# Kernel tuning notes

Measured on AMD Instinct MI355X. Metric: run time of the kernel, lower is better.

The kernel has to match this reference:

```python
import jax, jax.numpy as jnp
import numpy as np

BATCH = 131072
S = 128  # state_size == x_size


def setup_inputs() -> dict:
    key = jax.random.key(0)
    ks = jax.random.split(key, 7)
    std = 1.0 / np.sqrt(S).astype(np.float32)
    return {
        "x": jax.random.normal(ks[0], (BATCH, S), dtype=jnp.float32),
        "old_h": jax.random.normal(ks[1], (BATCH, S), dtype=jnp.float32),
        "W_x1": jax.random.normal(ks[2], (3, S, S), dtype=jnp.float32) * std,
        "W_x2": jax.random.normal(ks[3], (3, S, S), dtype=jnp.float32) * std,
        "W_h": jax.random.normal(ks[4], (6, S, S), dtype=jnp.float32) * std,
        "b": jnp.zeros((6, 1, S), dtype=jnp.float32),
        "mid": jax.random.normal(ks[5], (S, S), dtype=jnp.float32) * std,
    }


def reference(x, old_h, W_x1, W_x2, W_h, b, mid):
    sg = jax.nn.sigmoid
    # --- first GRU stage ---
    z = sg(x @ W_x1[0] + old_h @ W_h[0] + b[0])
    r = sg(x @ W_x1[1] + old_h @ W_h[1] + b[1])
    h_tilde = jnp.tanh(x @ W_x1[2] + (r * old_h) @ W_h[2] + b[2])
    mid_h = z * old_h + (1.0 - z) * h_tilde
    # mid_dropout with p=0 is identity
    mid_x = jax.nn.relu(mid_h @ mid)
    # --- second GRU stage (faithfully reuses W_h[0], b[0] as in source) ---
    z2 = sg(mid_x @ W_x2[0] + mid_h @ W_h[0] + b[0])
    r2 = sg(mid_x @ W_x2[1] + mid_h @ W_h[4] + b[4])
    h2_tilde = jnp.tanh(mid_x @ W_x2[2] + (r2 * mid_h) @ W_h[5] + b[5])
    h = z2 * mid_h + (1.0 - z2) * h2_tilde
    return (h,)
```

## Files before the change

kernel.cpp:

```cpp
#include <hip/hip_runtime.h>
#include <hip/hip_bf16.h>
#include <cstdint>


typedef __attribute__((ext_vector_type(8))) short bf16x8;
typedef __attribute__((ext_vector_type(4))) float f32x4;

#define S 128
#define BM 64
#define THREADS 512

#define SWZB(row) (((((row) & 7) ^ (((row) >> 2) & 2))) << 4)

__device__ __forceinline__ unsigned short f2bf(float f) {
    __hip_bfloat16 h = __float2bfloat16(f);
    return *reinterpret_cast<unsigned short*>(&h);
}
__device__ __forceinline__ float bf2f(unsigned short h) {
    unsigned int u = ((unsigned int)h) << 16;
    return __builtin_bit_cast(float, u);
}

__device__ __forceinline__ float fast_sig(float t) {
    float e = __expf(-t);
    return __builtin_amdgcn_rcpf(1.0f + e);
}
__device__ __forceinline__ float fast_tanh(float t) {
    float tc = fminf(fmaxf(t, -15.0f), 15.0f);
    float e = __expf(2.0f * tc);
    return (e - 1.0f) * __builtin_amdgcn_rcpf(e + 1.0f);
}

__global__ void pack_weights(const float* __restrict__ wx1,
                             const float* __restrict__ wx2,
                             const float* __restrict__ wh,
                             const float* __restrict__ mid,
                             unsigned short* __restrict__ dst) {
    int mat = blockIdx.x;
    const float* src;
    if (mat < 3)       src = wx1 + mat * (S * S);
    else if (mat < 6)  src = wx2 + (mat - 3) * (S * S);
    else if (mat < 12) src = wh  + (mat - 6) * (S * S);
    else               src = mid;
    int t = threadIdx.x;
    for (int f8 = 0; f8 < 8; ++f8) {
        int slot = f8 * 256 + t;
        int frag = slot >> 6;
        int lane = slot & 63;
        int kt  = frag >> 3;
        int ntg = frag & 7;
        int k0  = kt * 32 + (lane >> 4) * 8;
        int col = ntg * 16 + (lane & 15);
        unsigned int w[4];
#pragma unroll
        for (int p = 0; p < 4; ++p) {
            unsigned int lo = f2bf(src[(k0 + 2 * p) * S + col]);
            unsigned int hi = f2bf(src[(k0 + 2 * p + 1) * S + col]);
            w[p] = lo | (hi << 16);
        }
        uint4* d = (uint4*)(dst + (size_t)mat * (S * S) + frag * 512 + lane * 8);
        *d = make_uint4(w[0], w[1], w[2], w[3]);
    }
}

__device__ __forceinline__ bf16x8 lds_afrag(const unsigned short* s, int row, int kt, int lane) {
    int byte = row * 256 + kt * 64 + ((lane >> 4) << 4);
    byte ^= SWZB(row);
    return *(const bf16x8*)((const char*)s + byte);
}
__device__ __forceinline__ void st_bf(unsigned short* s, int row, int col, float v) {
    int byte = (row * 256 + col * 2) ^ SWZB(row);
    *(unsigned short*)((char*)s + byte) = f2bf(v);
}
__device__ __forceinline__ float ld_bf(const unsigned short* s, int row, int col) {
    int byte = (row * 256 + col * 2) ^ SWZB(row);
    return bf2f(*(const unsigned short*)((const char*)s + byte));
}

__device__ __forceinline__ void gemm_single(f32x4 (&acc)[4],
        const unsigned short* sA,
        const unsigned short* __restrict__ w0,
        int lane, int wc) {
    int rbase = lane & 15;
    __builtin_amdgcn_s_setprio(1);
#pragma unroll
    for (int kt = 0; kt < 4; ++kt) {
        bf16x8 a0[4];
#pragma unroll
        for (int m = 0; m < 4; ++m)
            a0[m] = lds_afrag(sA, rbase + m * 16, kt, lane);
        bf16x8 b0 = *(const bf16x8*)(w0 + (kt * 8 + wc) * 512 + lane * 8);
#pragma unroll
        for (int m = 0; m < 4; ++m)
            acc[m] = __builtin_amdgcn_mfma_f32_16x16x32_bf16(a0[m], b0, acc[m], 0, 0, 0);
    }
    __builtin_amdgcn_s_setprio(0);
}

__device__ __forceinline__ void gemm_pair2(f32x4 (&acc0)[4], f32x4 (&acc1)[4],
        const unsigned short* sA,
        const unsigned short* __restrict__ w0,
        const unsigned short* __restrict__ w1,
        int lane, int wc) {
    int rbase = lane & 15;
    __builtin_amdgcn_s_setprio(1);
#pragma unroll
    for (int kt = 0; kt < 4; ++kt) {
        bf16x8 a0[4];
#pragma unroll
        for (int m = 0; m < 4; ++m)
            a0[m] = lds_afrag(sA, rbase + m * 16, kt, lane);
        bf16x8 b0 = *(const bf16x8*)(w0 + (kt * 8 + wc) * 512 + lane * 8);
        bf16x8 b1 = *(const bf16x8*)(w1 + (kt * 8 + wc) * 512 + lane * 8);
#pragma unroll
        for (int m = 0; m < 4; ++m) {
            acc0[m] = __builtin_amdgcn_mfma_f32_16x16x32_bf16(a0[m], b0, acc0[m], 0, 0, 0);
            acc1[m] = __builtin_amdgcn_mfma_f32_16x16x32_bf16(a0[m], b1, acc1[m], 0, 0, 0);
        }
    }
    __builtin_amdgcn_s_setprio(0);
}

template <int OP>
__device__ __forceinline__ void finish(f32x4 (&acc)[4], float bc) {
#pragma unroll
    for (int m = 0; m < 4; ++m)
#pragma unroll
        for (int i = 0; i < 4; ++i) {
            float t = acc[m][i] + bc;
            acc[m][i] = (OP == 0) ? fast_sig(t) : fast_tanh(t);
        }
}

#define ZERO_ACC(A)                                           \
    _Pragma("unroll") for (int m = 0; m < 4; ++m)             \
        A[m] = (f32x4){0.f, 0.f, 0.f, 0.f};

#define FOR_COORDS(BODY)                                      \
    _Pragma("unroll") for (int m = 0; m < 4; ++m)             \
    _Pragma("unroll") for (int i = 0; i < 4; ++i) {           \
        int rt  = m * 16 + ((lane >> 4) << 2) + i;            \
        int col = wc * 16 + (lane & 15);                      \
        BODY                                                  \
    }

__global__ __launch_bounds__(THREADS, 4)
void dgru_main(const float* __restrict__ x, const float* __restrict__ old_h,
               const float* __restrict__ b, const unsigned short* __restrict__ wpk,
               float* __restrict__ out) {
    __shared__ __align__(16) unsigned short sx[S * BM];
    __shared__ __align__(16) unsigned short sh[S * BM];
    __shared__ __align__(16) unsigned short sg[S * BM];

    const int tid  = threadIdx.x;
    const int lane = tid & 63;
    const int wc   = tid >> 6;
    const long row0 = (long)blockIdx.x * BM;

    float bld[6];
#pragma unroll
    for (int j = 0; j < 6; ++j)
        bld[j] = b[j * S + wc * 16 + (lane & 15)];

#pragma unroll
    for (int it = 0; it < 2; ++it) {
        int slot = it * THREADS + tid;
        int row  = slot >> 4;
        int c8   = slot & 15;
        const float4* px = (const float4*)(x     + (row0 + row) * S + c8 * 8);
        const float4* ph = (const float4*)(old_h + (row0 + row) * S + c8 * 8);
        float4 v0 = px[0], v1 = px[1];
        float4 u0 = ph[0], u1 = ph[1];
        int byte = (row * 256 + c8 * 16) ^ SWZB(row);
        uint4 wx, wh;
        wx.x = (unsigned)f2bf(v0.x) | ((unsigned)f2bf(v0.y) << 16);
        wx.y = (unsigned)f2bf(v0.z) | ((unsigned)f2bf(v0.w) << 16);
        wx.z = (unsigned)f2bf(v1.x) | ((unsigned)f2bf(v1.y) << 16);
        wx.w = (unsigned)f2bf(v1.z) | ((unsigned)f2bf(v1.w) << 16);
        wh.x = (unsigned)f2bf(u0.x) | ((unsigned)f2bf(u0.y) << 16);
        wh.y = (unsigned)f2bf(u0.z) | ((unsigned)f2bf(u0.w) << 16);
        wh.z = (unsigned)f2bf(u1.x) | ((unsigned)f2bf(u1.y) << 16);
        wh.w = (unsigned)f2bf(u1.z) | ((unsigned)f2bf(u1.w) << 16);
        *(uint4*)((char*)sx + byte) = wx;
        *(uint4*)((char*)sh + byte) = wh;
    }
    __syncthreads();

#define WP(m) (wpk + (size_t)(m) * (S * S))

    float oh[4][4];
    float mh[4][4];

    f32x4 zz[4]; ZERO_ACC(zz);
    {
        f32x4 rr[4]; ZERO_ACC(rr);
        gemm_pair2(zz, rr, sx, WP(0), WP(1), lane, wc);
        gemm_pair2(zz, rr, sh, WP(6), WP(7), lane, wc);
        finish<0>(zz, bld[0]);
        finish<0>(rr, bld[1]);
        FOR_COORDS({
            oh[m][i] = ld_bf(sh, rt, col);
            st_bf(sg, rt, col, rr[m][i] * oh[m][i]);
        })
    }
    __syncthreads();

    {
        f32x4 ht[4]; ZERO_ACC(ht);
        gemm_single(ht, sx, WP(2), lane, wc);
        gemm_single(ht, sg, WP(8), lane, wc);
        finish<1>(ht, bld[2]);
        FOR_COORDS({
            float z = zz[m][i];
            mh[m][i] = z * oh[m][i] + (1.0f - z) * ht[m][i];
            st_bf(sh, rt, col, mh[m][i]);
        })
    }
    __syncthreads();

    {
        f32x4 mx[4]; ZERO_ACC(mx);
        gemm_single(mx, sh, WP(12), lane, wc);
        FOR_COORDS({
            float v = mx[m][i];
            st_bf(sx, rt, col, v > 0.0f ? v : 0.0f);
        })
    }
    __syncthreads();

    f32x4 z2[4]; ZERO_ACC(z2);
    {
        f32x4 r2[4]; ZERO_ACC(r2);
        gemm_pair2(z2, r2, sx, WP(3), WP(4), lane, wc);
        gemm_pair2(z2, r2, sh, WP(6), WP(10), lane, wc);
        finish<0>(z2, bld[0]);
        finish<0>(r2, bld[4]);
        FOR_COORDS({
            st_bf(sg, rt, col, r2[m][i] * mh[m][i]);
        })
    }
    __syncthreads();

    {
        f32x4 h2[4]; ZERO_ACC(h2);
        gemm_single(h2, sx, WP(5), lane, wc);
        gemm_single(h2, sg, WP(11), lane, wc);
        finish<1>(h2, bld[5]);
        FOR_COORDS({
            float z = z2[m][i];
            st_bf(sh, rt, col, z * mh[m][i] + (1.0f - z) * h2[m][i]);
        })
    }
    __syncthreads();

#pragma unroll
    for (int it = 0; it < 2; ++it) {
        int slot = it * THREADS + tid;
        int row  = slot >> 4;
        int c8   = slot & 15;
        int byte = (row * 256 + c8 * 16) ^ SWZB(row);
        bf16x8 v = *(const bf16x8*)((const char*)sh + byte);
        float4 f0, f1;
        f0.x = bf2f((unsigned short)v[0]); f0.y = bf2f((unsigned short)v[1]);
        f0.z = bf2f((unsigned short)v[2]); f0.w = bf2f((unsigned short)v[3]);
        f1.x = bf2f((unsigned short)v[4]); f1.y = bf2f((unsigned short)v[5]);
        f1.z = bf2f((unsigned short)v[6]); f1.w = bf2f((unsigned short)v[7]);
        float4* po = (float4*)(out + (row0 + row) * S + c8 * 8);
        po[0] = f0;
        po[1] = f1;
    }
}

extern "C" void kernel_launch(void* const* d_in, const int* in_sizes, int n_in,
                              void* d_out, int out_size, void* d_ws, size_t ws_size,
                              hipStream_t stream) {
    const float* x     = (const float*)d_in[0];
    const float* old_h = (const float*)d_in[1];
    const float* W_x1  = (const float*)d_in[2];
    const float* W_x2  = (const float*)d_in[3];
    const float* W_h   = (const float*)d_in[4];
    const float* b     = (const float*)d_in[5];
    const float* mid   = (const float*)d_in[6];
    float* out = (float*)d_out;
    unsigned short* wpk = (unsigned short*)d_ws;

    int batch = in_sizes[0] / S;

    pack_weights<<<13, 256, 0, stream>>>(W_x1, W_x2, W_h, mid, wpk);
    dgru_main<<<batch / BM, THREADS, 0, stream>>>(x, old_h, b, wpk, out);
}
```

Before: 112.1 us.

## Switch GEMMs to 32x32x16 MFMA with 2x4 wave tiling

Replaces the 16x16x32 MFMA tiling, where each wave owned a 64x16 output strip, with 32x32x16 MFMA where each wave owns a 32x32 tile in a 2x4 wave grid. The weight packing layout changes to match the new B-fragment shape. Each wave now needs one A fragment per k-step instead of four, which cuts LDS reads and B-fragment global loads per MFMA. Intermediate old_h and mid_h values are re-read from LDS as bf16 instead of being held in registers, which lowers register pressure but uses the rounded bf16 copies and adds LDS traffic.

```diff
diff --git a/kernel.cpp b/kernel.cpp
--- a/kernel.cpp
+++ b/kernel.cpp
@@ -4,7 +4,7 @@
 
 
 typedef __attribute__((ext_vector_type(8))) short bf16x8;
-typedef __attribute__((ext_vector_type(4))) float f32x4;
+typedef __attribute__((ext_vector_type(16))) float f32x16;
 
 #define S 128
 #define BM 64
@@ -47,10 +47,10 @@
         int slot = f8 * 256 + t;
         int frag = slot >> 6;
         int lane = slot & 63;
-        int kt  = frag >> 3;
-        int ntg = frag & 7;
-        int k0  = kt * 32 + (lane >> 4) * 8;
-        int col = ntg * 16 + (lane & 15);
+        int kt  = frag >> 2;
+        int ng  = frag & 3;
+        int k0  = kt * 16 + (lane >> 5) * 8;
+        int col = ng * 32 + (lane & 31);
         unsigned int w[4];
 #pragma unroll
         for (int p = 0; p < 4; ++p) {
@@ -63,85 +63,71 @@
     }
 }
 
-__device__ __forceinline__ bf16x8 lds_afrag(const unsigned short* s, int row, int kt, int lane) {
-    int byte = row * 256 + kt * 64 + ((lane >> 4) << 4);
-    byte ^= SWZB(row);
-    return *(const bf16x8*)((const char*)s + byte);
-}
 __device__ __forceinline__ void st_bf(unsigned short* s, int row, int col, float v) {
-    int byte = (row * 256 + col * 2) ^ SWZB(row);
+    int byte = row * 256 + ((col * 2) ^ SWZB(row));
     *(unsigned short*)((char*)s + byte) = f2bf(v);
 }
 __device__ __forceinline__ float ld_bf(const unsigned short* s, int row, int col) {
-    int byte = (row * 256 + col * 2) ^ SWZB(row);
+    int byte = row * 256 + ((col * 2) ^ SWZB(row));
     return bf2f(*(const unsigned short*)((const char*)s + byte));
 }
 
-__device__ __forceinline__ void gemm_single(f32x4 (&acc)[4],
-        const unsigned short* sA,
-        const unsigned short* __restrict__ w0,
-        int lane, int wc) {
-    int rbase = lane & 15;
+__device__ __forceinline__ void gemm32(f32x16& acc, const unsigned short* sA,
+        const unsigned short* __restrict__ w0, int lane, int wr, int wcg) {
+    int row  = wr * 32 + (lane & 31);
+    int rb   = row * 256;
+    int half = (lane >> 5) << 4;
+    int swz  = SWZB(row);
+    const unsigned short* wb = w0 + wcg * 512 + lane * 8;
     __builtin_amdgcn_s_setprio(1);
 #pragma unroll
-    for (int kt = 0; kt < 4; ++kt) {
-        bf16x8 a0[4];
-#pragma unroll
-        for (int m = 0; m < 4; ++m)
-            a0[m] = lds_afrag(sA, rbase + m * 16, kt, lane);
-        bf16x8 b0 = *(const bf16x8*)(w0 + (kt * 8 + wc) * 512 + lane * 8);
-#pragma unroll
-        for (int m = 0; m < 4; ++m)
-            acc[m] = __builtin_amdgcn_mfma_f32_16x16x32_bf16(a0[m], b0, acc[m], 0, 0, 0);
+    for (int kt = 0; kt < 8; ++kt) {
+        bf16x8 a = *(const bf16x8*)((const char*)sA + rb + (((kt << 5) | half) ^ swz));
+        bf16x8 b = *(const bf16x8*)(wb + kt * 2048);
+        acc = __builtin_amdgcn_mfma_f32_32x32x16_bf16(a, b, acc, 0, 0, 0);
     }
     __builtin_amdgcn_s_setprio(0);
 }
 
-__device__ __forceinline__ void gemm_pair2(f32x4 (&acc0)[4], f32x4 (&acc1)[4],
+__device__ __forceinline__ void gemm32_pair(f32x16& acc0, f32x16& acc1,
         const unsigned short* sA,
         const unsigned short* __restrict__ w0,
         const unsigned short* __restrict__ w1,
-        int lane, int wc) {
-    int rbase = lane & 15;
+        int lane, int wr, int wcg) {
+    int row  = wr * 32 + (lane & 31);
+    int rb   = row * 256;
+    int half = (lane >> 5) << 4;
+    int swz  = SWZB(row);
+    const unsigned short* wb0 = w0 + wcg * 512 + lane * 8;
+    const unsigned short* wb1 = w1 + wcg * 512 + lane * 8;
     __builtin_amdgcn_s_setprio(1);
 #pragma unroll
-    for (int kt = 0; kt < 4; ++kt) {
-        bf16x8 a0[4];
-#pragma unroll
-        for (int m = 0; m < 4; ++m)
-            a0[m] = lds_afrag(sA, rbase + m * 16, kt, lane);
-        bf16x8 b0 = *(const bf16x8*)(w0 + (kt * 8 + wc) * 512 + lane * 8);
-        bf16x8 b1 = *(const bf16x8*)(w1 + (kt * 8 + wc) * 512 + lane * 8);
-#pragma unroll
-        for (int m = 0; m < 4; ++m) {
-            acc0[m] = __builtin_amdgcn_mfma_f32_16x16x32_bf16(a0[m], b0, acc0[m], 0, 0, 0);
-            acc1[m] = __builtin_amdgcn_mfma_f32_16x16x32_bf16(a0[m], b1, acc1[m], 0, 0, 0);
-        }
+    for (int kt = 0; kt < 8; ++kt) {
+        bf16x8 a  = *(const bf16x8*)((const char*)sA + rb + (((kt << 5) | half) ^ swz));
+        bf16x8 b0 = *(const bf16x8*)(wb0 + kt * 2048);
+        bf16x8 b1 = *(const bf16x8*)(wb1 + kt * 2048);
+        acc0 = __builtin_amdgcn_mfma_f32_32x32x16_bf16(a, b0, acc0, 0, 0, 0);
+        acc1 = __builtin_amdgcn_mfma_f32_32x32x16_bf16(a, b1, acc1, 0, 0, 0);
     }
     __builtin_amdgcn_s_setprio(0);
 }
 
 template <int OP>
-__device__ __forceinline__ void finish(f32x4 (&acc)[4], float bc) {
-#pragma unroll
-    for (int m = 0; m < 4; ++m)
-#pragma unroll
-        for (int i = 0; i < 4; ++i) {
-            float t = acc[m][i] + bc;
-            acc[m][i] = (OP == 0) ? fast_sig(t) : fast_tanh(t);
-        }
-}
-
-#define ZERO_ACC(A)                                           \
-    _Pragma("unroll") for (int m = 0; m < 4; ++m)             \
-        A[m] = (f32x4){0.f, 0.f, 0.f, 0.f};
-
-#define FOR_COORDS(BODY)                                      \
-    _Pragma("unroll") for (int m = 0; m < 4; ++m)             \
-    _Pragma("unroll") for (int i = 0; i < 4; ++i) {           \
-        int rt  = m * 16 + ((lane >> 4) << 2) + i;            \
-        int col = wc * 16 + (lane & 15);                      \
-        BODY                                                  \
+__device__ __forceinline__ void finish(f32x16& acc, float bc) {
+#pragma unroll
+    for (int e = 0; e < 16; ++e) {
+        float t = acc[e] + bc;
+        acc[e] = (OP == 0) ? fast_sig(t) : fast_tanh(t);
+    }
+}
+
+#define ZERO_ACC(A) { _Pragma("unroll") for (int e = 0; e < 16; ++e) A[e] = 0.f; }
+
+#define FOR_COORDS(BODY)                                              \
+    _Pragma("unroll") for (int rg = 0; rg < 16; ++rg) {               \
+        int rt  = wr * 32 + (rg & 3) + ((rg >> 2) << 3) + ((lane >> 5) << 2); \
+        int col = wcg * 32 + (lane & 31);                             \
+        BODY                                                          \
     }
 
 __global__ __launch_bounds__(THREADS, 4)
@@ -154,13 +140,15 @@
 
     const int tid  = threadIdx.x;
     const int lane = tid & 63;
-    const int wc   = tid >> 6;
+    const int wid  = tid >> 6;
+    const int wr   = wid >> 2;
+    const int wcg  = wid & 3;
     const long row0 = (long)blockIdx.x * BM;
 
     float bld[6];
 #pragma unroll
     for (int j = 0; j < 6; ++j)
-        bld[j] = b[j * S + wc * 16 + (lane & 15)];
+        bld[j] = b[j * S + wcg * 32 + (lane & 31)];
 
 #pragma unroll
     for (int it = 0; it < 2; ++it) {
@@ -171,7 +159,7 @@
         const float4* ph = (const float4*)(old_h + (row0 + row) * S + c8 * 8);
         float4 v0 = px[0], v1 = px[1];
         float4 u0 = ph[0], u1 = ph[1];
-        int byte = (row * 256 + c8 * 16) ^ SWZB(row);
+        int byte = row * 256 + ((c8 * 16) ^ SWZB(row));
         uint4 wx, wh;
         wx.x = (unsigned)f2bf(v0.x) | ((unsigned)f2bf(v0.y) << 16);
         wx.y = (unsigned)f2bf(v0.z) | ((unsigned)f2bf(v0.w) << 16);
@@ -188,67 +176,66 @@
 
 #define WP(m) (wpk + (size_t)(m) * (S * S))
 
-    float oh[4][4];
-    float mh[4][4];
-
-    f32x4 zz[4]; ZERO_ACC(zz);
-    {
-        f32x4 rr[4]; ZERO_ACC(rr);
-        gemm_pair2(zz, rr, sx, WP(0), WP(1), lane, wc);
-        gemm_pair2(zz, rr, sh, WP(6), WP(7), lane, wc);
+    f32x16 zz; ZERO_ACC(zz);
+    {
+        f32x16 rr; ZERO_ACC(rr);
+        gemm32_pair(zz, rr, sx, WP(0), WP(1), lane, wr, wcg);
+        gemm32_pair(zz, rr, sh, WP(6), WP(7), lane, wr, wcg);
         finish<0>(zz, bld[0]);
         finish<0>(rr, bld[1]);
         FOR_COORDS({
-            oh[m][i] = ld_bf(sh, rt, col);
-            st_bf(sg, rt, col, rr[m][i] * oh[m][i]);
-        })
-    }
-    __syncthreads();
-
-    {
-        f32x4 ht[4]; ZERO_ACC(ht);
-        gemm_single(ht, sx, WP(2), lane, wc);
-        gemm_single(ht, sg, WP(8), lane, wc);
+            float oh = ld_bf(sh, rt, col);
+            st_bf(sg, rt, col, rr[rg] * oh);
+        })
+    }
+    __syncthreads();
+
+    {
+        f32x16 ht; ZERO_ACC(ht);
+        gemm32(ht, sx, WP(2), lane, wr, wcg);
+        gemm32(ht, sg, WP(8), lane, wr, wcg);
         finish<1>(ht, bld[2]);
         FOR_COORDS({
-            float z = zz[m][i];
-            mh[m][i] = z * oh[m][i] + (1.0f - z) * ht[m][i];
-            st_bf(sh, rt, col, mh[m][i]);
-        })
-    }
-    __syncthreads();
-
-    {
-        f32x4 mx[4]; ZERO_ACC(mx);
-        gemm_single(mx, sh, WP(12), lane, wc);
-        FOR_COORDS({
-            float v = mx[m][i];
+            float oh = ld_bf(sh, rt, col);
+            float z  = zz[rg];
+            st_bf(sh, rt, col, z * oh + (1.0f - z) * ht[rg]);
+        })
+    }
+    __syncthreads();
+
+    {
+        f32x16 mx; ZERO_ACC(mx);
+        gemm32(mx, sh, WP(12), lane, wr, wcg);
+        FOR_COORDS({
+            float v = mx[rg];
             st_bf(sx, rt, col, v > 0.0f ? v : 0.0f);
         })
     }
     __syncthreads();
 
-    f32x4 z2[4]; ZERO_ACC(z2);
-    {
-        f32x4 r2[4]; ZERO_ACC(r2);
-        gemm_pair2(z2, r2, sx, WP(3), WP(4), lane, wc);
-        gemm_pair2(z2, r2, sh, WP(6), WP(10), lane, wc);
+    f32x16 z2; ZERO_ACC(z2);
+    {
+        f32x16 r2; ZERO_ACC(r2);
+        gemm32_pair(z2, r2, sx, WP(3), WP(4), lane, wr, wcg);
+        gemm32_pair(z2, r2, sh, WP(6), WP(10), lane, wr, wcg);
         finish<0>(z2, bld[0]);
         finish<0>(r2, bld[4]);
         FOR_COORDS({
-            st_bf(sg, rt, col, r2[m][i] * mh[m][i]);
-        })
-    }
-    __syncthreads();
-
-    {
-        f32x4 h2[4]; ZERO_ACC(h2);
-        gemm_single(h2, sx, WP(5), lane, wc);
-        gemm_single(h2, sg, WP(11), lane, wc);
+            float mhv = ld_bf(sh, rt, col);
+            st_bf(sg, rt, col, r2[rg] * mhv);
+        })
+    }
+    __syncthreads();
+
+    {
+        f32x16 h2; ZERO_ACC(h2);
+        gemm32(h2, sx, WP(5), lane, wr, wcg);
+        gemm32(h2, sg, WP(11), lane, wr, wcg);
         finish<1>(h2, bld[5]);
         FOR_COORDS({
-            float z = z2[m][i];
-            st_bf(sh, rt, col, z * mh[m][i] + (1.0f - z) * h2[m][i]);
+            float z   = z2[rg];
+            float mhv = ld_bf(sh, rt, col);
+            st_bf(sh, rt, col, z * mhv + (1.0f - z) * h2[rg]);
         })
     }
     __syncthreads();
@@ -258,7 +245,7 @@
         int slot = it * THREADS + tid;
         int row  = slot >> 4;
         int c8   = slot & 15;
-        int byte = (row * 256 + c8 * 16) ^ SWZB(row);
+        int byte = row * 256 + ((c8 * 16) ^ SWZB(row));
         bf16x8 v = *(const bf16x8*)((const char*)sh + byte);
         float4 f0, f1;
         f0.x = bf2f((unsigned short)v[0]); f0.y = bf2f((unsigned short)v[1]);
```

Result: faster. 108.5 us (-3.2%).

## Process two 64-row sub-tiles per block to reuse weight fetches across rows

Applied to the files above, without the earlier changes.

Doubles the block's row count to 128 by splitting it into two 64-row sub-tiles that each GEMM stage loops over, with shared-memory buffers doubled to match. The aim is to amortize weight loads and block launch overhead over more rows. Intermediate mid_h and old_h values are re-read from LDS instead of being held in registers, which lowers register pressure. The cost is double the LDS per block, launch bounds dropping from 4 to 2 blocks, and the extra LDS reads.

```diff
diff --git a/kernel.cpp b/kernel.cpp
--- a/kernel.cpp
+++ b/kernel.cpp
@@ -7,7 +7,8 @@
 typedef __attribute__((ext_vector_type(4))) float f32x4;
 
 #define S 128
-#define BM 64
+#define TM 64
+#define BM 128
 #define THREADS 512
 
 #define SWZB(row) (((((row) & 7) ^ (((row) >> 2) & 2))) << 4)
@@ -144,13 +145,13 @@
         BODY                                                  \
     }
 
-__global__ __launch_bounds__(THREADS, 4)
+__global__ __launch_bounds__(THREADS, 2)
 void dgru_main(const float* __restrict__ x, const float* __restrict__ old_h,
                const float* __restrict__ b, const unsigned short* __restrict__ wpk,
                float* __restrict__ out) {
-    __shared__ __align__(16) unsigned short sx[S * BM];
-    __shared__ __align__(16) unsigned short sh[S * BM];
-    __shared__ __align__(16) unsigned short sg[S * BM];
+    __shared__ __align__(16) unsigned short sx[2][S * TM];
+    __shared__ __align__(16) unsigned short sh[2][S * TM];
+    __shared__ __align__(16) unsigned short sg[2][S * TM];
 
     const int tid  = threadIdx.x;
     const int lane = tid & 63;
@@ -163,15 +164,17 @@
         bld[j] = b[j * S + wc * 16 + (lane & 15)];
 
 #pragma unroll
-    for (int it = 0; it < 2; ++it) {
+    for (int it = 0; it < 4; ++it) {
         int slot = it * THREADS + tid;
         int row  = slot >> 4;
+        int tl   = row >> 6;
+        int r    = row & 63;
         int c8   = slot & 15;
         const float4* px = (const float4*)(x     + (row0 + row) * S + c8 * 8);
         const float4* ph = (const float4*)(old_h + (row0 + row) * S + c8 * 8);
         float4 v0 = px[0], v1 = px[1];
         float4 u0 = ph[0], u1 = ph[1];
-        int byte = (row * 256 + c8 * 16) ^ SWZB(row);
+        int byte = (r * 256 + c8 * 16) ^ SWZB(r);
         uint4 wx, wh;
         wx.x = (unsigned)f2bf(v0.x) | ((unsigned)f2bf(v0.y) << 16);
         wx.y = (unsigned)f2bf(v0.z) | ((unsigned)f2bf(v0.w) << 16);
@@ -181,85 +184,93 @@
         wh.y = (unsigned)f2bf(u0.z) | ((unsigned)f2bf(u0.w) << 16);
         wh.z = (unsigned)f2bf(u1.x) | ((unsigned)f2bf(u1.y) << 16);
         wh.w = (unsigned)f2bf(u1.z) | ((unsigned)f2bf(u1.w) << 16);
-        *(uint4*)((char*)sx + byte) = wx;
-        *(uint4*)((char*)sh + byte) = wh;
+        *(uint4*)((char*)sx[tl] + byte) = wx;
+        *(uint4*)((char*)sh[tl] + byte) = wh;
     }
     __syncthreads();
 
 #define WP(m) (wpk + (size_t)(m) * (S * S))
 
-    float oh[4][4];
-    float mh[4][4];
-
-    f32x4 zz[4]; ZERO_ACC(zz);
-    {
+    f32x4 zz[2][4];
+#pragma unroll
+    for (int tl = 0; tl < 2; ++tl) {
+        ZERO_ACC(zz[tl]);
         f32x4 rr[4]; ZERO_ACC(rr);
-        gemm_pair2(zz, rr, sx, WP(0), WP(1), lane, wc);
-        gemm_pair2(zz, rr, sh, WP(6), WP(7), lane, wc);
-        finish<0>(zz, bld[0]);
+        gemm_pair2(zz[tl], rr, sx[tl], WP(0), WP(1), lane, wc);
+        gemm_pair2(zz[tl], rr, sh[tl], WP(6), WP(7), lane, wc);
+        finish<0>(zz[tl], bld[0]);
         finish<0>(rr, bld[1]);
         FOR_COORDS({
-            oh[m][i] = ld_bf(sh, rt, col);
-            st_bf(sg, rt, col, rr[m][i] * oh[m][i]);
-        })
-    }
-    __syncthreads();
-
-    {
+            float oh = ld_bf(sh[tl], rt, col);
+            st_bf(sg[tl], rt, col, rr[m][i] * oh);
+        })
+    }
+    __syncthreads();
+
+#pragma unroll
+    for (int tl = 0; tl < 2; ++tl) {
         f32x4 ht[4]; ZERO_ACC(ht);
-        gemm_single(ht, sx, WP(2), lane, wc);
-        gemm_single(ht, sg, WP(8), lane, wc);
+        gemm_single(ht, sx[tl], WP(2), lane, wc);
+        gemm_single(ht, sg[tl], WP(8), lane, wc);
         finish<1>(ht, bld[2]);
         FOR_COORDS({
-            float z = zz[m][i];
-            mh[m][i] = z * oh[m][i] + (1.0f - z) * ht[m][i];
-            st_bf(sh, rt, col, mh[m][i]);
-        })
-    }
-    __syncthreads();
-
-    {
+            float oh = ld_bf(sh[tl], rt, col);
+            float z  = zz[tl][m][i];
+            st_bf(sh[tl], rt, col, z * oh + (1.0f - z) * ht[m][i]);
+        })
+    }
+    __syncthreads();
+
+#pragma unroll
+    for (int tl = 0; tl < 2; ++tl) {
         f32x4 mx[4]; ZERO_ACC(mx);
-        gemm_single(mx, sh, WP(12), lane, wc);
+        gemm_single(mx, sh[tl], WP(12), lane, wc);
         FOR_COORDS({
             float v = mx[m][i];
-            st_bf(sx, rt, col, v > 0.0f ? v : 0.0f);
-        })
-    }
-    __syncthreads();
-
-    f32x4 z2[4]; ZERO_ACC(z2);
-    {
+            st_bf(sx[tl], rt, col, v > 0.0f ? v : 0.0f);
+        })
+    }
+    __syncthreads();
+
+    f32x4 z2[2][4];
+#pragma unroll
+    for (int tl = 0; tl < 2; ++tl) {
+        ZERO_ACC(z2[tl]);
         f32x4 r2[4]; ZERO_ACC(r2);
-        gemm_pair2(z2, r2, sx, WP(3), WP(4), lane, wc);
-        gemm_pair2(z2, r2, sh, WP(6), WP(10), lane, wc);
-        finish<0>(z2, bld[0]);
+        gemm_pair2(z2[tl], r2, sx[tl], WP(3), WP(4), lane, wc);
+        gemm_pair2(z2[tl], r2, sh[tl], WP(6), WP(10), lane, wc);
+        finish<0>(z2[tl], bld[0]);
         finish<0>(r2, bld[4]);
         FOR_COORDS({
-            st_bf(sg, rt, col, r2[m][i] * mh[m][i]);
-        })
-    }
-    __syncthreads();
-
-    {
+            float mhv = ld_bf(sh[tl], rt, col);
+            st_bf(sg[tl], rt, col, r2[m][i] * mhv);
+        })
+    }
+    __syncthreads();
+
+#pragma unroll
+    for (int tl = 0; tl < 2; ++tl) {
         f32x4 h2[4]; ZERO_ACC(h2);
-        gemm_single(h2, sx, WP(5), lane, wc);
-        gemm_single(h2, sg, WP(11), lane, wc);
+        gemm_single(h2, sx[tl], WP(5), lane, wc);
+        gemm_single(h2, sg[tl], WP(11), lane, wc);
         finish<1>(h2, bld[5]);
         FOR_COORDS({
-            float z = z2[m][i];
-            st_bf(sh, rt, col, z * mh[m][i] + (1.0f - z) * h2[m][i]);
-        })
-    }
-    __syncthreads();
-
-#pragma unroll
-    for (int it = 0; it < 2; ++it) {
+            float z   = z2[tl][m][i];
+            float mhv = ld_bf(sh[tl], rt, col);
+            st_bf(sh[tl], rt, col, z * mhv + (1.0f - z) * h2[m][i]);
+        })
+    }
+    __syncthreads();
+
+#pragma unroll
+    for (int it = 0; it < 4; ++it) {
         int slot = it * THREADS + tid;
         int row  = slot >> 4;
+        int tl   = row >> 6;
+        int r    = row & 63;
         int c8   = slot & 15;
-        int byte = (row * 256 + c8 * 16) ^ SWZB(row);
-        bf16x8 v = *(const bf16x8*)((const char*)sh + byte);
+        int byte = (r * 256 + c8 * 16) ^ SWZB(r);
+        bf16x8 v = *(const bf16x8*)((const char*)sh[tl] + byte);
         float4 f0, f1;
         f0.x = bf2f((unsigned short)v[0]); f0.y = bf2f((unsigned short)v[1]);
         f0.z = bf2f((unsigned short)v[2]); f0.w = bf2f((unsigned short)v[3]);
```

New measurement: 124.8 us. +11.3%, slower.
